# Kernel optimization log

Measured on AMD Instinct MI355X. Metric: run time of the kernel, lower is better.

Reference implementation:

```python
import jax, jax.numpy as jnp
import numpy as np

D_MODEL = 1024
HEADS = 16
D_K = D_MODEL // HEADS
NEG_INF = -1e10


def setup_inputs() -> dict:
    key = jax.random.key(0)
    ks = jax.random.split(key, 10)
    n, s = 2, 2048
    inp = {
        "value": jax.random.normal(ks[0], (n, s, D_MODEL), dtype=jnp.float32),
        "key": jax.random.normal(ks[1], (n, s, D_MODEL), dtype=jnp.float32),
        "query": jax.random.normal(ks[2], (n, s, D_MODEL), dtype=jnp.float32),
        "mask": jax.random.randint(ks[3], (n, 1, s, s), 0, 2, dtype=jnp.int32),
        # torch.nn.Linear weights are [out, in]; y = x @ W.T (+ b)
        "Wq": jax.random.normal(ks[4], (D_MODEL, D_MODEL), dtype=jnp.float32) * (D_MODEL ** -0.5),
        "Wk": jax.random.normal(ks[5], (D_MODEL, D_MODEL), dtype=jnp.float32) * (D_MODEL ** -0.5),
        "Wv": jax.random.normal(ks[6], (D_MODEL, D_MODEL), dtype=jnp.float32) * (D_MODEL ** -0.5),
        "Wo": jax.random.normal(ks[7], (D_MODEL, D_MODEL), dtype=jnp.float32) * (D_MODEL ** -0.5),
        "bo": jax.random.normal(ks[8], (D_MODEL,), dtype=jnp.float32) * 0.01,
    }
    return inp


def reference(value, key, query, mask, Wq, Wk, Wv, Wo, bo):
    n, q_len, _ = query.shape
    # projections (Linear, no bias): x @ W.T
    q = (query @ Wq.T).reshape(n, q_len, HEADS, D_K)
    k = (key @ Wk.T).reshape(n, key.shape[1], HEADS, D_K)
    v = (value @ Wv.T).reshape(n, value.shape[1], HEADS, D_K)
    scores = jnp.einsum('nqhd,nkhd->nhqk', q, k)  # [n,h,q,k]
    scores = jnp.where(mask == 0, jnp.float32(NEG_INF), scores)
    attn = jax.nn.softmax(scores / jnp.sqrt(jnp.float32(D_K)), axis=-1)
    out = jnp.einsum('nhql,nlhd->nqhd', attn, v).reshape(n, q_len, D_MODEL)
    return out @ Wo.T + bo
```

## Files before the change

### kernel.cpp

```cpp
#include <hip/hip_runtime.h>
#include <hip/hip_bf16.h>
#include <stdint.h>

#define SEQ     2048
#define NBATCH  2
#define DMODEL  1024
#define NH      16
#define DKH     64

typedef __bf16 bf16;
typedef __attribute__((ext_vector_type(8))) __bf16 bf16x8;
typedef __attribute__((ext_vector_type(4))) __bf16 bf16x4;
typedef __attribute__((ext_vector_type(4))) float  f32x4;

static __device__ __forceinline__ f32x4 mfma16(bf16x8 a, bf16x8 b, f32x4 c) {
    return __builtin_amdgcn_mfma_f32_16x16x32_bf16(a, b, c, 0, 0, 0);
}

typedef const __attribute__((address_space(1))) void* gas_cptr;
typedef __attribute__((address_space(3))) void*       las_ptr;
#define GLDS16(g, l) __builtin_amdgcn_global_load_lds((gas_cptr)(g), (las_ptr)(l), 16, 0, 0)

__global__ __launch_bounds__(256) void cvt_all_k(const float* __restrict__ q,
                                                 const float* __restrict__ k,
                                                 const float* __restrict__ v,
                                                 const float* __restrict__ wq,
                                                 const float* __restrict__ wk,
                                                 const float* __restrict__ wv,
                                                 const float* __restrict__ wo,
                                                 bf16* __restrict__ qb, bf16* __restrict__ kb,
                                                 bf16* __restrict__ vb, bf16* __restrict__ wqb,
                                                 bf16* __restrict__ wkb, bf16* __restrict__ wvb,
                                                 bf16* __restrict__ wob) {
    const float* src; bf16* dst; int n4;
    const int NX4 = (NBATCH * SEQ * DMODEL) / 4, NW4 = (DMODEL * DMODEL) / 4;
    switch (blockIdx.y) {
        case 0: src = q;  dst = qb;  n4 = NX4; break;
        case 1: src = k;  dst = kb;  n4 = NX4; break;
        case 2: src = v;  dst = vb;  n4 = NX4; break;
        case 3: src = wq; dst = wqb; n4 = NW4; break;
        case 4: src = wk; dst = wkb; n4 = NW4; break;
        case 5: src = wv; dst = wvb; n4 = NW4; break;
        default: src = wo; dst = wob; n4 = NW4; break;
    }
    int stride = gridDim.x * blockDim.x;
    for (int i = blockIdx.x * blockDim.x + threadIdx.x; i < n4; i += stride) {
        f32x4 f = ((const f32x4*)src)[i];
        bf16x4 o;
#pragma unroll
        for (int j = 0; j < 4; j++) o[j] = (bf16)f[j];
        ((bf16x4*)dst)[i] = o;
    }
}

__global__ __launch_bounds__(256) void pack_mask_k(const int* __restrict__ mask,
                                                   unsigned long long* __restrict__ bits,
                                                   int nwords) {
    int wave  = (blockIdx.x * blockDim.x + threadIdx.x) >> 6;
    int lane  = threadIdx.x & 63;
    int nwtot = (gridDim.x * blockDim.x) >> 6;
    for (int w = wave; w < nwords; w += nwtot) {
        int m = mask[(size_t)w * 64 + lane];
        unsigned long long b = __ballot(m != 0);
        if (lane == 0) bits[w] = b;
    }
}

__global__ __launch_bounds__(256) void qkv_gemm(const bf16* __restrict__ Xq,
                                                const bf16* __restrict__ Xk,
                                                const bf16* __restrict__ Xv,
                                                const bf16* __restrict__ Wq,
                                                const bf16* __restrict__ Wk,
                                                const bf16* __restrict__ Wv,
                                                bf16* __restrict__ Qo,
                                                bf16* __restrict__ Ko,
                                                bf16* __restrict__ Vto) {
    __shared__ bf16 As[128 * 32], Bs[128 * 32];
    const int z = blockIdx.z;
    const bf16* A = (z == 0) ? Xq : (z == 1) ? Xk : Xv;
    const bf16* W = (z == 0) ? Wq : (z == 1) ? Wk : Wv;
    const int bm = blockIdx.x * 128, bn = blockIdx.y * 128;
    const int tid = threadIdx.x, wave = tid >> 6, lane = tid & 63;
    const int wm = wave >> 1, wn = wave & 1, lo = lane & 15, hi = lane >> 4;

    const int r0 = wave * 32 + (lane >> 2);
    const int c8 = (lane & 3) * 8;
    const bf16* Ag = A + (size_t)(bm + r0) * DMODEL + c8;
    const bf16* Bg = W + (size_t)(bn + r0) * DMODEL + c8;
    bf16* lA = &As[wave * 1024];
    bf16* lB = &Bs[wave * 1024];

    f32x4 acc[4][4];
#pragma unroll
    for (int i = 0; i < 4; i++)
#pragma unroll
        for (int j = 0; j < 4; j++) acc[i][j] = 0.0f;

    for (int k0 = 0; k0 < DMODEL; k0 += 32) {
        __syncthreads();
        GLDS16(Ag + k0, lA);
        GLDS16(Ag + k0 + (size_t)16 * DMODEL, lA + 512);
        GLDS16(Bg + k0, lB);
        GLDS16(Bg + k0 + (size_t)16 * DMODEL, lB + 512);
        __syncthreads();

        bf16x8 a[4], b[4];
#pragma unroll
        for (int t = 0; t < 4; t++) {
            a[t] = *(const bf16x8*)&As[(wm * 64 + t * 16 + lo) * 32 + hi * 8];
            b[t] = *(const bf16x8*)&Bs[(wn * 64 + t * 16 + lo) * 32 + hi * 8];
        }
#pragma unroll
        for (int tm = 0; tm < 4; tm++)
#pragma unroll
            for (int tn = 0; tn < 4; tn++)
                acc[tm][tn] = mfma16(a[tm], b[tn], acc[tm][tn]);
    }

    if (z < 2) {
        bf16* O = (z == 0) ? Qo : Ko;
#pragma unroll
        for (int tm = 0; tm < 4; tm++)
#pragma unroll
            for (int tn = 0; tn < 4; tn++)
#pragma unroll
                for (int r = 0; r < 4; r++) {
                    int m = bm + wm * 64 + tm * 16 + hi * 4 + r;
                    int o = bn + wn * 64 + tn * 16 + lo;
                    int nidx = m >> 11, sq = m & 2047;
                    int hh = o >> 6, d = o & 63;
                    O[(((size_t)nidx * NH + hh) * SEQ + sq) * DKH + d] = (bf16)acc[tm][tn][r];
                }
    } else {
#pragma unroll
        for (int tm = 0; tm < 4; tm++)
#pragma unroll
            for (int tn = 0; tn < 4; tn++)
#pragma unroll
                for (int r = 0; r < 4; r++) {
                    int m = bm + wm * 64 + tm * 16 + hi * 4 + r;
                    int o = bn + wn * 64 + tn * 16 + lo;
                    int nidx = m >> 11, sq = m & 2047;
                    int hh = o >> 6, d = o & 63;
                    Vto[(((size_t)nidx * NH + hh) * DKH + d) * SEQ + sq] = (bf16)acc[tm][tn][r];
                }
    }
}

__global__ __launch_bounds__(256, 3) void attn_k(const bf16* __restrict__ Q,
                                                 const bf16* __restrict__ K,
                                                 const bf16* __restrict__ Vt,
                                                 const unsigned long long* __restrict__ mbits,
                                                 bf16* __restrict__ Oattn) {
    __shared__ bf16 Ks[2][64 * 72];
    __shared__ bf16 Vs[2][64 * 72];
    __shared__ bf16 Ps[64 * 72];

    const int bid = blockIdx.x;
    const int xcd = bid & 7, j = bid >> 3;
    const int hd = xcd * 4 + (j & 3);
    const int qb = j >> 2;
    const int n = hd >> 4, h = hd & 15;

    const int tid = threadIdx.x, wave = tid >> 6, lane = tid & 63;
    const int lo = lane & 15, hi = lane >> 4;

    const size_t headoff = (size_t)hd * SEQ * DKH;
    const bf16* Qh = Q + headoff;
    const bf16* Kh = K + headoff;
    const bf16* Vh = Vt + headoff;

    const int qrow = qb * 64 + wave * 16 + lo;
    const bf16x8 aq0 = *(const bf16x8*)(Qh + (size_t)qrow * DKH + hi * 8);
    const bf16x8 aq1 = *(const bf16x8*)(Qh + (size_t)qrow * DKH + 32 + hi * 8);

    bf16x8 ones;
#pragma unroll
    for (int i = 0; i < 8; i++) ones[i] = (bf16)1.0f;

    f32x4 oacc[4];
#pragma unroll
    for (int t = 0; t < 4; t++) oacc[t] = 0.0f;
    f32x4 lacc; lacc = 0.0f;

    const unsigned long long* mb = mbits + ((size_t)n * SEQ + qb * 64 + wave * 16) * (SEQ / 64);
    const float c = 0.18033688f;

    const int srow = tid >> 3, sseg = tid & 7;
    const bf16* Kg = Kh + (size_t)srow * DKH + sseg * 8;
    const bf16* Vg = Vh + (size_t)srow * SEQ + sseg * 8;
    const int si0 = srow * 72 + sseg * 8;
    const int si1 = (srow + 32) * 72 + sseg * 8;

    bf16x8 rk0 = *(const bf16x8*)(Kg);
    bf16x8 rk1 = *(const bf16x8*)(Kg + (size_t)32 * DKH);
    bf16x8 rv0 = *(const bf16x8*)(Vg);
    bf16x8 rv1 = *(const bf16x8*)(Vg + (size_t)32 * SEQ);
    *(bf16x8*)&Ks[0][si0] = rk0;
    *(bf16x8*)&Ks[0][si1] = rk1;
    *(bf16x8*)&Vs[0][si0] = rv0;
    *(bf16x8*)&Vs[0][si1] = rv1;
    rk0 = *(const bf16x8*)(Kg + (size_t)64 * DKH);
    rk1 = *(const bf16x8*)(Kg + (size_t)96 * DKH);
    rv0 = *(const bf16x8*)(Vg + 64);
    rv1 = *(const bf16x8*)(Vg + (size_t)32 * SEQ + 64);
    __syncthreads();

    int p = 0;
    for (int k0 = 0; k0 < SEQ; k0 += 64) {
        unsigned long long w64[4];
#pragma unroll
        for (int r = 0; r < 4; r++) w64[r] = mb[(size_t)(hi * 4 + r) * (SEQ / 64) + (k0 >> 6)];

        f32x4 s[4];
#pragma unroll
        for (int tn = 0; tn < 4; tn++) {
            const int kr = (tn * 16 + lo) * 72;
            bf16x8 b0 = *(const bf16x8*)&Ks[p][kr + hi * 8];
            bf16x8 b1 = *(const bf16x8*)&Ks[p][kr + 32 + hi * 8];
            f32x4 z4; z4 = 0.0f;
            z4 = mfma16(aq0, b0, z4);
            z4 = mfma16(aq1, b1, z4);
            s[tn] = z4;
        }

        if (k0 + 64 < SEQ) {
            *(bf16x8*)&Ks[p ^ 1][si0] = rk0;
            *(bf16x8*)&Ks[p ^ 1][si1] = rk1;
            *(bf16x8*)&Vs[p ^ 1][si0] = rv0;
            *(bf16x8*)&Vs[p ^ 1][si1] = rv1;
            if (k0 + 128 < SEQ) {
                rk0 = *(const bf16x8*)(Kg + (size_t)(k0 + 128) * DKH);
                rk1 = *(const bf16x8*)(Kg + (size_t)(k0 + 160) * DKH);
                rv0 = *(const bf16x8*)(Vg + k0 + 128);
                rv1 = *(const bf16x8*)(Vg + (size_t)32 * SEQ + k0 + 128);
            }
        }

#pragma unroll
        for (int r = 0; r < 4; r++) {
            unsigned wlo = (unsigned)(w64[r] >> lo);
            unsigned whi = (unsigned)(w64[r] >> (lo + 32));
#pragma unroll
            for (int tn = 0; tn < 4; tn++) {
                unsigned bit = ((tn < 2 ? wlo : whi) >> ((tn & 1) * 16)) & 1u;
                float pv = exp2f(s[tn][r] * c);
                pv = bit ? pv : 0.0f;
                Ps[(wave * 16 + hi * 4 + r) * 72 + tn * 16 + lo] = (bf16)pv;
            }
        }
        asm volatile("s_waitcnt lgkmcnt(0)" ::: "memory");

        bf16x8 ap0 = *(const bf16x8*)&Ps[(wave * 16 + lo) * 72 + hi * 8];
        bf16x8 ap1 = *(const bf16x8*)&Ps[(wave * 16 + lo) * 72 + 32 + hi * 8];
#pragma unroll
        for (int td = 0; td < 4; td++) {
            bf16x8 b0 = *(const bf16x8*)&Vs[p][(td * 16 + lo) * 72 + hi * 8];
            bf16x8 b1 = *(const bf16x8*)&Vs[p][(td * 16 + lo) * 72 + 32 + hi * 8];
            oacc[td] = mfma16(ap0, b0, oacc[td]);
            oacc[td] = mfma16(ap1, b1, oacc[td]);
        }
        lacc = mfma16(ap0, ones, lacc);
        lacc = mfma16(ap1, ones, lacc);

        __syncthreads();
        p ^= 1;
    }

#pragma unroll
    for (int td = 0; td < 4; td++)
#pragma unroll
        for (int r = 0; r < 4; r++) {
            int q = qb * 64 + wave * 16 + hi * 4 + r;
            int d = td * 16 + lo;
            Oattn[((size_t)n * SEQ + q) * DMODEL + h * 64 + d] = (bf16)(oacc[td][r] / lacc[r]);
        }
}

__global__ __launch_bounds__(256) void out_gemm(const bf16* __restrict__ A,
                                                const bf16* __restrict__ W,
                                                const float* __restrict__ bias,
                                                float* __restrict__ Out) {
    __shared__ bf16 As[128 * 32], Bs[128 * 32];
    const int bm = blockIdx.x * 128, bn = blockIdx.y * 128;
    const int tid = threadIdx.x, wave = tid >> 6, lane = tid & 63;
    const int wm = wave >> 1, wn = wave & 1, lo = lane & 15, hi = lane >> 4;

    const int r0 = wave * 32 + (lane >> 2);
    const int c8 = (lane & 3) * 8;
    const bf16* Ag = A + (size_t)(bm + r0) * DMODEL + c8;
    const bf16* Bg = W + (size_t)(bn + r0) * DMODEL + c8;
    bf16* lA = &As[wave * 1024];
    bf16* lB = &Bs[wave * 1024];

    f32x4 acc[4][4];
#pragma unroll
    for (int i = 0; i < 4; i++)
#pragma unroll
        for (int j = 0; j < 4; j++) acc[i][j] = 0.0f;

    for (int k0 = 0; k0 < DMODEL; k0 += 32) {
        __syncthreads();
        GLDS16(Ag + k0, lA);
        GLDS16(Ag + k0 + (size_t)16 * DMODEL, lA + 512);
        GLDS16(Bg + k0, lB);
        GLDS16(Bg + k0 + (size_t)16 * DMODEL, lB + 512);
        __syncthreads();

        bf16x8 a[4], b[4];
#pragma unroll
        for (int t = 0; t < 4; t++) {
            a[t] = *(const bf16x8*)&As[(wm * 64 + t * 16 + lo) * 32 + hi * 8];
            b[t] = *(const bf16x8*)&Bs[(wn * 64 + t * 16 + lo) * 32 + hi * 8];
        }
#pragma unroll
        for (int tm = 0; tm < 4; tm++)
#pragma unroll
            for (int tn = 0; tn < 4; tn++)
                acc[tm][tn] = mfma16(a[tm], b[tn], acc[tm][tn]);
    }

#pragma unroll
    for (int tm = 0; tm < 4; tm++)
#pragma unroll
        for (int tn = 0; tn < 4; tn++) {
            int o = bn + wn * 64 + tn * 16 + lo;
            float bv = bias[o];
#pragma unroll
            for (int r = 0; r < 4; r++) {
                int m = bm + wm * 64 + tm * 16 + hi * 4 + r;
                Out[(size_t)m * DMODEL + o] = acc[tm][tn][r] + bv;
            }
        }
}

extern "C" void kernel_launch(void* const* d_in, const int* in_sizes, int n_in,
                              void* d_out, int out_size, void* d_ws, size_t ws_size,
                              hipStream_t stream) {
    const float* value = (const float*)d_in[0];
    const float* key   = (const float*)d_in[1];
    const float* query = (const float*)d_in[2];
    const int*   mask  = (const int*)d_in[3];
    const float* Wq    = (const float*)d_in[4];
    const float* Wk    = (const float*)d_in[5];
    const float* Wv    = (const float*)d_in[6];
    const float* Wo    = (const float*)d_in[7];
    const float* bo    = (const float*)d_in[8];
    float* out = (float*)d_out;

    char* ws = (char*)d_ws;
    bf16* Qws = (bf16*)(ws);
    bf16* Kws = (bf16*)(ws + (8u  << 20));
    bf16* Vt  = (bf16*)(ws + (16u << 20));
    bf16* Xqb = (bf16*)(ws + (24u << 20));
    bf16* Xkb = (bf16*)(ws + (32u << 20));
    bf16* Xvb = (bf16*)(ws + (40u << 20));
    bf16* Wqb = (bf16*)(ws + (48u << 20));
    bf16* Wkb = (bf16*)(ws + (50u << 20));
    bf16* Wvb = (bf16*)(ws + (52u << 20));
    bf16* Wob = (bf16*)(ws + (54u << 20));
    unsigned long long* mbits = (unsigned long long*)(ws + (56u << 20));
    bf16* Aws = Xqb;

    cvt_all_k<<<dim3(1024, 7), 256, 0, stream>>>(query, key, value, Wq, Wk, Wv, Wo,
                                                 Xqb, Xkb, Xvb, Wqb, Wkb, Wvb, Wob);
    pack_mask_k<<<1024, 256, 0, stream>>>(mask, mbits, NBATCH * SEQ * (SEQ / 64));
    qkv_gemm<<<dim3(32, 8, 3), 256, 0, stream>>>(Xqb, Xkb, Xvb, Wqb, Wkb, Wvb, Qws, Kws, Vt);
    attn_k<<<1024, 256, 0, stream>>>(Qws, Kws, Vt, mbits, Aws);
    out_gemm<<<dim3(32, 8), 256, 0, stream>>>(Aws, Wob, bo, out);
}
```

Baseline: 311.8 us.

## Split attention key range in two with a merge kernel and higher occupancy

Attention blocks now each process half of the key sequence, doubling the grid, and write unnormalized partial outputs plus row sums; a new merge kernel sums the partials and normalizes. LDS double buffering is dropped and launch bounds raised to allow more resident blocks per CU. This targets poor tail utilization and low occupancy, at the cost of extra global traffic for partials, an additional launch, and lost load/compute overlap from single buffering.

```diff
diff --git a/kernel.cpp b/kernel.cpp
--- a/kernel.cpp
+++ b/kernel.cpp
@@ -147,19 +147,22 @@
     }
 }
 
-__global__ __launch_bounds__(256, 3) void attn_k(const bf16* __restrict__ Q,
+__global__ __launch_bounds__(256, 5) void attn_k(const bf16* __restrict__ Q,
                                                  const bf16* __restrict__ K,
                                                  const bf16* __restrict__ Vt,
                                                  const unsigned long long* __restrict__ mbits,
-                                                 bf16* __restrict__ Oattn) {
-    __shared__ bf16 Ks[2][64 * 72];
-    __shared__ bf16 Vs[2][64 * 72];
+                                                 bf16* __restrict__ Op0,
+                                                 bf16* __restrict__ Op1,
+                                                 float* __restrict__ Lp) {
+    __shared__ bf16 Ks[64 * 72];
+    __shared__ bf16 Vs[64 * 72];
     __shared__ bf16 Ps[64 * 72];
 
     const int bid = blockIdx.x;
     const int xcd = bid & 7, j = bid >> 3;
     const int hd = xcd * 4 + (j & 3);
-    const int qb = j >> 2;
+    const int qb = (j >> 2) & 31;
+    const int ks = j >> 7;
     const int n = hd >> 4, h = hd & 15;
 
     const int tid = threadIdx.x, wave = tid >> 6, lane = tid & 63;
@@ -186,28 +189,31 @@
     const unsigned long long* mb = mbits + ((size_t)n * SEQ + qb * 64 + wave * 16) * (SEQ / 64);
     const float c = 0.18033688f;
 
+    const int kbeg = ks * 1024, kend = kbeg + 1024;
+
     const int srow = tid >> 3, sseg = tid & 7;
     const bf16* Kg = Kh + (size_t)srow * DKH + sseg * 8;
     const bf16* Vg = Vh + (size_t)srow * SEQ + sseg * 8;
-    const int si0 = srow * 72 + sseg * 8;
-    const int si1 = (srow + 32) * 72 + sseg * 8;
-
-    bf16x8 rk0 = *(const bf16x8*)(Kg);
-    bf16x8 rk1 = *(const bf16x8*)(Kg + (size_t)32 * DKH);
-    bf16x8 rv0 = *(const bf16x8*)(Vg);
-    bf16x8 rv1 = *(const bf16x8*)(Vg + (size_t)32 * SEQ);
-    *(bf16x8*)&Ks[0][si0] = rk0;
-    *(bf16x8*)&Ks[0][si1] = rk1;
-    *(bf16x8*)&Vs[0][si0] = rv0;
-    *(bf16x8*)&Vs[0][si1] = rv1;
-    rk0 = *(const bf16x8*)(Kg + (size_t)64 * DKH);
-    rk1 = *(const bf16x8*)(Kg + (size_t)96 * DKH);
-    rv0 = *(const bf16x8*)(Vg + 64);
-    rv1 = *(const bf16x8*)(Vg + (size_t)32 * SEQ + 64);
-    __syncthreads();
-
-    int p = 0;
-    for (int k0 = 0; k0 < SEQ; k0 += 64) {
+
+    bf16x8 rk0 = *(const bf16x8*)(Kg + (size_t)kbeg * DKH);
+    bf16x8 rk1 = *(const bf16x8*)(Kg + (size_t)(kbeg + 32) * DKH);
+    bf16x8 rv0 = *(const bf16x8*)(Vg + kbeg);
+    bf16x8 rv1 = *(const bf16x8*)(Vg + (size_t)32 * SEQ + kbeg);
+
+    for (int k0 = kbeg; k0 < kend; k0 += 64) {
+        __syncthreads();
+        *(bf16x8*)&Ks[srow * 72 + sseg * 8]        = rk0;
+        *(bf16x8*)&Ks[(srow + 32) * 72 + sseg * 8] = rk1;
+        *(bf16x8*)&Vs[srow * 72 + sseg * 8]        = rv0;
+        *(bf16x8*)&Vs[(srow + 32) * 72 + sseg * 8] = rv1;
+        if (k0 + 64 < kend) {
+            rk0 = *(const bf16x8*)(Kg + (size_t)(k0 + 64) * DKH);
+            rk1 = *(const bf16x8*)(Kg + (size_t)(k0 + 96) * DKH);
+            rv0 = *(const bf16x8*)(Vg + k0 + 64);
+            rv1 = *(const bf16x8*)(Vg + (size_t)32 * SEQ + k0 + 64);
+        }
+        __syncthreads();
+
         unsigned long long w64[4];
 #pragma unroll
         for (int r = 0; r < 4; r++) w64[r] = mb[(size_t)(hi * 4 + r) * (SEQ / 64) + (k0 >> 6)];
@@ -216,25 +222,12 @@
 #pragma unroll
         for (int tn = 0; tn < 4; tn++) {
             const int kr = (tn * 16 + lo) * 72;
-            bf16x8 b0 = *(const bf16x8*)&Ks[p][kr + hi * 8];
-            bf16x8 b1 = *(const bf16x8*)&Ks[p][kr + 32 + hi * 8];
+            bf16x8 b0 = *(const bf16x8*)&Ks[kr + hi * 8];
+            bf16x8 b1 = *(const bf16x8*)&Ks[kr + 32 + hi * 8];
             f32x4 z4; z4 = 0.0f;
             z4 = mfma16(aq0, b0, z4);
             z4 = mfma16(aq1, b1, z4);
             s[tn] = z4;
-        }
-
-        if (k0 + 64 < SEQ) {
-            *(bf16x8*)&Ks[p ^ 1][si0] = rk0;
-            *(bf16x8*)&Ks[p ^ 1][si1] = rk1;
-            *(bf16x8*)&Vs[p ^ 1][si0] = rv0;
-            *(bf16x8*)&Vs[p ^ 1][si1] = rv1;
-            if (k0 + 128 < SEQ) {
-                rk0 = *(const bf16x8*)(Kg + (size_t)(k0 + 128) * DKH);
-                rk1 = *(const bf16x8*)(Kg + (size_t)(k0 + 160) * DKH);
-                rv0 = *(const bf16x8*)(Vg + k0 + 128);
-                rv1 = *(const bf16x8*)(Vg + (size_t)32 * SEQ + k0 + 128);
-            }
         }
 
 #pragma unroll
@@ -255,26 +248,50 @@
         bf16x8 ap1 = *(const bf16x8*)&Ps[(wave * 16 + lo) * 72 + 32 + hi * 8];
 #pragma unroll
         for (int td = 0; td < 4; td++) {
-            bf16x8 b0 = *(const bf16x8*)&Vs[p][(td * 16 + lo) * 72 + hi * 8];
-            bf16x8 b1 = *(const bf16x8*)&Vs[p][(td * 16 + lo) * 72 + 32 + hi * 8];
+            bf16x8 b0 = *(const bf16x8*)&Vs[(td * 16 + lo) * 72 + hi * 8];
+            bf16x8 b1 = *(const bf16x8*)&Vs[(td * 16 + lo) * 72 + 32 + hi * 8];
             oacc[td] = mfma16(ap0, b0, oacc[td]);
             oacc[td] = mfma16(ap1, b1, oacc[td]);
         }
         lacc = mfma16(ap0, ones, lacc);
         lacc = mfma16(ap1, ones, lacc);
-
-        __syncthreads();
-        p ^= 1;
-    }
-
+    }
+
+    bf16* Op = ks ? Op1 : Op0;
 #pragma unroll
     for (int td = 0; td < 4; td++)
 #pragma unroll
         for (int r = 0; r < 4; r++) {
             int q = qb * 64 + wave * 16 + hi * 4 + r;
             int d = td * 16 + lo;
-            Oattn[((size_t)n * SEQ + q) * DMODEL + h * 64 + d] = (bf16)(oacc[td][r] / lacc[r]);
-        }
+            Op[((size_t)n * SEQ + q) * DMODEL + h * 64 + d] = (bf16)oacc[td][r];
+        }
+    if (lo == 0) {
+#pragma unroll
+        for (int r = 0; r < 4; r++) {
+            int q = qb * 64 + wave * 16 + hi * 4 + r;
+            Lp[(size_t)ks * (NBATCH * NH * SEQ) + ((size_t)(n * NH + h) * SEQ) + q] = lacc[r];
+        }
+    }
+}
+
+__global__ __launch_bounds__(256) void merge_k(const bf16* __restrict__ o0,
+                                               const bf16* __restrict__ o1,
+                                               const float* __restrict__ lp,
+                                               bf16* __restrict__ Aout) {
+    int t = blockIdx.x * blockDim.x + threadIdx.x;
+    int q = t >> 7;
+    int h = (t >> 3) & 15;
+    int n = q >> 11;
+    bf16x8 a = ((const bf16x8*)o0)[t];
+    bf16x8 b = ((const bf16x8*)o1)[t];
+    int li = (n * NH + h) * SEQ + (q & 2047);
+    float l = lp[li] + lp[NBATCH * NH * SEQ + li];
+    float rl = 1.0f / l;
+    bf16x8 o;
+#pragma unroll
+    for (int i = 0; i < 8; i++) o[i] = (bf16)(((float)a[i] + (float)b[i]) * rl);
+    ((bf16x8*)Aout)[t] = o;
 }
 
 __global__ __launch_bounds__(256) void out_gemm(const bf16* __restrict__ A,
@@ -360,12 +377,16 @@
     bf16* Wvb = (bf16*)(ws + (52u << 20));
     bf16* Wob = (bf16*)(ws + (54u << 20));
     unsigned long long* mbits = (unsigned long long*)(ws + (56u << 20));
-    bf16* Aws = Xqb;
+    bf16*  Op0 = Xqb;
+    bf16*  Op1 = Xkb;
+    bf16*  Aws = Xvb;
+    float* Lp  = (float*)Wqb;
 
     cvt_all_k<<<dim3(1024, 7), 256, 0, stream>>>(query, key, value, Wq, Wk, Wv, Wo,
                                                  Xqb, Xkb, Xvb, Wqb, Wkb, Wvb, Wob);
     pack_mask_k<<<1024, 256, 0, stream>>>(mask, mbits, NBATCH * SEQ * (SEQ / 64));
     qkv_gemm<<<dim3(32, 8, 3), 256, 0, stream>>>(Xqb, Xkb, Xvb, Wqb, Wkb, Wvb, Qws, Kws, Vt);
-    attn_k<<<1024, 256, 0, stream>>>(Qws, Kws, Vt, mbits, Aws);
+    attn_k<<<2048, 256, 0, stream>>>(Qws, Kws, Vt, mbits, Op0, Op1, Lp);
+    merge_k<<<2048, 256, 0, stream>>>(Op0, Op1, Lp, Aws);
     out_gemm<<<dim3(32, 8), 256, 0, stream>>>(Aws, Wob, bo, out);
 }
```

New measurement: 299.7 us. -3.9%, faster.
